# Optimization experiments

Hardware: AMD Instinct MI355X
Metric: run time of the kernel (lower is better)

Reference implementation:

```python
import jax, jax.numpy as jnp
import numpy as np

D_MODEL = 256
NHEAD = 8
HEAD_DIM = D_MODEL // NHEAD
TOP_K = 16
TEMP = 0.1
INF = 1e9
LAYER_NAMES = ['self', 'cross'] * 4


def _ln(x, g, b):
    m = jnp.mean(x, -1, keepdims=True)
    v = jnp.mean((x - m) ** 2, -1, keepdims=True)
    return (x - m) * jax.lax.rsqrt(v + 1e-5) * g + b


def _conf(f0, f1, m0, m1):
    # feats scaled by 1/sqrt(C) each, then /temperature -> sim / (C * TEMP)
    c = f0.shape[-1]
    sim = jnp.einsum('nlc,nsc->nls', f0, f1) / (c * TEMP)
    valid = m0[:, :, None] & m1[:, None, :]
    sim = jnp.where(valid, sim, -INF)
    return jax.nn.softmax(sim, axis=1) * jax.nn.softmax(sim, axis=2)


def _select(feat, conf, k):
    _, idx = jax.lax.top_k(conf, k)                 # [N, L, K]
    return jax.vmap(lambda f, i: f[i])(feat, idx)    # [N, L, K, C]


def _lin_attn(q, k, v, qm):
    # LoFTR LinearAttention: elu feature map, kv_mask is None here
    Q = jax.nn.elu(q) + 1.0
    K = jax.nn.elu(k) + 1.0
    if qm is not None:
        Q = Q * qm[:, :, None, None]
    vlen = v.shape[1]
    v = v / vlen
    KV = jnp.einsum('nshd,nshv->nhdv', K, v)
    Z = 1.0 / (jnp.einsum('nlhd,nhd->nlh', Q, K.sum(1)) + 1e-6)
    return jnp.einsum('nlhd,nhdv,nlh->nlhv', Q, KV, Z) * vlen


def _layer(x, src, xm, p):
    Wq, Wk, Wv, Wm, W1, W2, g1, b1, g2, b2 = p
    bs = x.shape[0]
    q = (x @ Wq).reshape(bs, -1, NHEAD, HEAD_DIM)
    k = (src @ Wk).reshape(bs, -1, NHEAD, HEAD_DIM)
    v = (src @ Wv).reshape(bs, -1, NHEAD, HEAD_DIM)
    msg = _lin_attn(q, k, v, xm)
    msg = msg.reshape(bs, -1, D_MODEL) @ Wm
    msg = _ln(msg, g1, b1)
    msg = jax.nn.relu(jnp.concatenate([x, msg], -1) @ W1) @ W2
    msg = _ln(msg, g2, b2)
    return x + msg


def _forward(feat0, feat1, mask0, mask1, Wq, Wk, Wv, Wm, W1, W2, g1, b1, g2, b2):
    N, L, C = feat0.shape
    S = feat1.shape[1]
    K = TOP_K
    m0f = mask0.reshape(N * L, 1).astype(feat0.dtype)
    m1f = mask1.reshape(N * S, 1).astype(feat0.dtype)
    for i, name in enumerate(LAYER_NAMES):
        p = (Wq[i], Wk[i], Wv[i], Wm[i], W1[i], W2[i], g1[i], b1[i], g2[i], b2[i])
        f0 = feat0.reshape(N * L, 1, C)
        f1 = feat1.reshape(N * S, 1, C)
        if name == 'self':
            s00 = _select(feat0, _conf(feat0, feat0, mask0, mask0), K).reshape(N * L, K, C)
            s11 = _select(feat1, _conf(feat1, feat1, mask1, mask1), K).reshape(N * S, K, C)
            feat0 = _layer(f0, s00, m0f, p).reshape(N, L, C)
            feat1 = _layer(f1, s11, m1f, p).reshape(N, S, C)
        else:
            c01 = _conf(feat0, feat1, mask0, mask1)
            s01 = _select(feat1, c01, K).reshape(N * L, K, C)
            s10 = _select(feat0, jnp.swapaxes(c01, 1, 2), K).reshape(N * S, K, C)
            feat0 = _layer(f0, s01, m0f, p).reshape(N, L, C)
            feat1 = _layer(f1, s10, m1f, p).reshape(N, S, C)
    return feat0, feat1


def setup_inputs() -> dict:
    key = jax.random.key(0)
    ks = jax.random.split(key, 10)
    N, L, S, C = 2, 4800, 4800, D_MODEL
    nl = len(LAYER_NAMES)
    w = 0.05
    return {
        'feat0': jax.random.normal(ks[0], (N, L, C), jnp.float32),
        'feat1': jax.random.normal(ks[1], (N, S, C), jnp.float32),
        'mask0': jnp.ones((N, L), jnp.bool_),
        'mask1': jnp.ones((N, S), jnp.bool_),
        'Wq': jax.random.normal(ks[2], (nl, C, C), jnp.float32) * w,
        'Wk': jax.random.normal(ks[3], (nl, C, C), jnp.float32) * w,
        'Wv': jax.random.normal(ks[4], (nl, C, C), jnp.float32) * w,
        'Wm': jax.random.normal(ks[5], (nl, C, C), jnp.float32) * w,
        'W1': jax.random.normal(ks[6], (nl, 2 * C, 2 * C), jnp.float32) * w,
        'W2': jax.random.normal(ks[7], (nl, 2 * C, C), jnp.float32) * w,
        'g1': jnp.ones((nl, C), jnp.float32),
        'b1': jnp.zeros((nl, C), jnp.float32),
        'g2': jnp.ones((nl, C), jnp.float32),
        'b2': jnp.zeros((nl, C), jnp.float32),
    }


def reference(feat0, feat1, mask0, mask1, Wq, Wk, Wv, Wm, W1, W2, g1, b1, g2, b2):
    return _forward(feat0, feat1, mask0, mask1, Wq, Wk, Wv, Wm, W1, W2, g1, b1, g2, b2)
```

## Files before the change

kernel.cpp:

```cpp
#include <hip/hip_runtime.h>

#define LLEN 4800
#define CDIM 256
#define NCH 8
#define CHROWS 600
#define SUBR 75

template <int MODE>
__global__ __launch_bounds__(256) void gemm_nt_sim(
    const float* __restrict__ A, const float* __restrict__ B,
    float* __restrict__ C, float* __restrict__ CT)
{
  const int bxi = blockIdx.x, byi = blockIdx.y;
  if (MODE == 1 && bxi < byi) return;
  const int bm = byi * 128, bn = bxi * 128;
  __shared__ float pool[MODE ? 8512 : 4224];
  float (*As)[132] = (float (*)[132])pool;
  float (*Bs)[132] = (float (*)[132])(pool + 2112);
  const int t = threadIdx.x;
  const int tx = t & 15, ty = t >> 4;
  const int lr = t >> 2, lk = (t & 3) * 4;
  float acc[8][8] = {};
  for (int k0 = 0; k0 < CDIM; k0 += 16) {
#pragma unroll
    for (int h = 0; h < 2; ++h) {
      const int row = lr + h * 64;
      const int ga = min(bm + row, LLEN - 1);
      const int gb = min(bn + row, LLEN - 1);
      const float4 a = *(const float4*)&A[(size_t)ga * CDIM + k0 + lk];
      const float4 b = *(const float4*)&B[(size_t)gb * CDIM + k0 + lk];
      As[lk + 0][row] = a.x; As[lk + 1][row] = a.y;
      As[lk + 2][row] = a.z; As[lk + 3][row] = a.w;
      Bs[lk + 0][row] = b.x; Bs[lk + 1][row] = b.y;
      Bs[lk + 2][row] = b.z; Bs[lk + 3][row] = b.w;
    }
    __syncthreads();
#pragma unroll
    for (int k = 0; k < 16; ++k) {
      const float4 a0 = *(const float4*)&As[k][ty * 4];
      const float4 a1 = *(const float4*)&As[k][64 + ty * 4];
      const float4 b0 = *(const float4*)&Bs[k][tx * 4];
      const float4 b1 = *(const float4*)&Bs[k][64 + tx * 4];
      const float av[8] = {a0.x, a0.y, a0.z, a0.w, a1.x, a1.y, a1.z, a1.w};
      const float bv[8] = {b0.x, b0.y, b0.z, b0.w, b1.x, b1.y, b1.z, b1.w};
#pragma unroll
      for (int i = 0; i < 8; ++i)
#pragma unroll
        for (int j = 0; j < 8; ++j) acc[i][j] += av[i] * bv[j];
    }
    __syncthreads();
  }
  const float sc = 1.f / 25.6f;
#pragma unroll
  for (int i = 0; i < 8; ++i) {
    const int row = bm + ((i < 4) ? ty * 4 + i : 64 + ty * 4 + (i - 4));
    if (row < LLEN) {
      const int c0 = bn + tx * 4;
      if (c0 < LLEN) {
        float4 o = {acc[i][0] * sc, acc[i][1] * sc, acc[i][2] * sc, acc[i][3] * sc};
        *(float4*)(C + (size_t)row * LLEN + c0) = o;
      }
      if (c0 + 64 < LLEN) {
        float4 o = {acc[i][4] * sc, acc[i][5] * sc, acc[i][6] * sc, acc[i][7] * sc};
        *(float4*)(C + (size_t)row * LLEN + c0 + 64) = o;
      }
    }
  }
  if (MODE == 0) return;
  if (MODE == 1 && bxi == byi) return;
  float* D = (MODE == 1) ? C : CT;
  float (*Ts)[133] = (float (*)[133])pool;
  for (int chunk = 0; chunk < 2; ++chunk) {
    __syncthreads();
#pragma unroll
    for (int i = 0; i < 8; ++i) {
      const int rl = (i < 4) ? ty * 4 + i : 64 + ty * 4 + (i - 4);
#pragma unroll
      for (int jj = 0; jj < 4; ++jj)
        Ts[tx * 4 + jj][rl] = acc[i][chunk * 4 + jj] * sc;
    }
    __syncthreads();
    const int cl = t >> 2, seg = t & 3;
    const int drow = bn + chunk * 64 + cl;
    if (drow < LLEN) {
#pragma unroll
      for (int q = 0; q < 8; ++q) {
        const int dcol = bm + seg * 32 + q * 4;
        if (dcol < LLEN) {
          const int b = seg * 32 + q * 4;
          float4 o = {Ts[cl][b], Ts[cl][b + 1], Ts[cl][b + 2], Ts[cl][b + 3]};
          *(float4*)(D + (size_t)drow * LLEN + dcol) = o;
        }
      }
    }
  }
}

template <int ACT>
__global__ __launch_bounds__(256) void gemm_nn(
    const float* __restrict__ A1, const float* __restrict__ A2,
    const float* __restrict__ B, float* __restrict__ C, int N, int K, int KA1)
{
  const int bm = blockIdx.y * 128, bn = blockIdx.x * 128;
  __shared__ float As[16][132];
  __shared__ float Bs[16][132];
  const int t = threadIdx.x;
  const int tx = t & 15, ty = t >> 4;
  const int lr = t >> 2, lk = (t & 3) * 4;
  const int bc = (t & 31) * 4, bk = t >> 5;
  float acc[8][8] = {};
  for (int k0 = 0; k0 < K; k0 += 16) {
    const float* Ap; int kloc, lda;
    if (k0 < KA1) { Ap = A1; kloc = k0; lda = KA1; }
    else          { Ap = A2; kloc = k0 - KA1; lda = K - KA1; }
#pragma unroll
    for (int h = 0; h < 2; ++h) {
      const int row = lr + h * 64;
      const float4 a = *(const float4*)&Ap[(size_t)(bm + row) * lda + kloc + lk];
      As[lk + 0][row] = a.x; As[lk + 1][row] = a.y;
      As[lk + 2][row] = a.z; As[lk + 3][row] = a.w;
    }
#pragma unroll
    for (int h = 0; h < 2; ++h) {
      const int kr = bk + h * 8;
      *(float4*)&Bs[kr][bc] = *(const float4*)&B[(size_t)(k0 + kr) * N + bn + bc];
    }
    __syncthreads();
#pragma unroll
    for (int k = 0; k < 16; ++k) {
      const float4 a0 = *(const float4*)&As[k][ty * 4];
      const float4 a1 = *(const float4*)&As[k][64 + ty * 4];
      const float4 b0 = *(const float4*)&Bs[k][tx * 4];
      const float4 b1 = *(const float4*)&Bs[k][64 + tx * 4];
      const float av[8] = {a0.x, a0.y, a0.z, a0.w, a1.x, a1.y, a1.z, a1.w};
      const float bv[8] = {b0.x, b0.y, b0.z, b0.w, b1.x, b1.y, b1.z, b1.w};
#pragma unroll
      for (int i = 0; i < 8; ++i)
#pragma unroll
        for (int j = 0; j < 8; ++j) acc[i][j] += av[i] * bv[j];
    }
    __syncthreads();
  }
#pragma unroll
  for (int i = 0; i < 8; ++i) {
    const int row = bm + ((i < 4) ? ty * 4 + i : 64 + ty * 4 + (i - 4));
    float4 o0 = {acc[i][0], acc[i][1], acc[i][2], acc[i][3]};
    float4 o1 = {acc[i][4], acc[i][5], acc[i][6], acc[i][7]};
    if (ACT == 1) {
      o0.x = fmaxf(o0.x, 0.f); o0.y = fmaxf(o0.y, 0.f);
      o0.z = fmaxf(o0.z, 0.f); o0.w = fmaxf(o0.w, 0.f);
      o1.x = fmaxf(o1.x, 0.f); o1.y = fmaxf(o1.y, 0.f);
      o1.z = fmaxf(o1.z, 0.f); o1.w = fmaxf(o1.w, 0.f);
    }
    *(float4*)(C + (size_t)row * N + bn + tx * 4) = o0;
    *(float4*)(C + (size_t)row * N + bn + tx * 4 + 64) = o1;
  }
}

__global__ __launch_bounds__(256) void gemm_qkv(
    const float* __restrict__ F,
    const float* __restrict__ Wq, const float* __restrict__ Wk, const float* __restrict__ Wv,
    float* __restrict__ qb, float* __restrict__ kb, float* __restrict__ vb)
{
  const int bm = blockIdx.y * 128;
  const int gn = blockIdx.x * 128;
  const int sel = gn >> 8;
  const int bn = gn & 255;
  const float* __restrict__ B = (sel == 0) ? Wq : (sel == 1) ? Wk : Wv;
  float* __restrict__ C = (sel == 0) ? qb : (sel == 1) ? kb : vb;
  __shared__ float As[16][132];
  __shared__ float Bs[16][132];
  const int t = threadIdx.x;
  const int tx = t & 15, ty = t >> 4;
  const int lr = t >> 2, lk = (t & 3) * 4;
  const int bc = (t & 31) * 4, bk = t >> 5;
  float acc[8][8] = {};
  for (int k0 = 0; k0 < CDIM; k0 += 16) {
#pragma unroll
    for (int h = 0; h < 2; ++h) {
      const int row = lr + h * 64;
      const float4 a = *(const float4*)&F[(size_t)(bm + row) * CDIM + k0 + lk];
      As[lk + 0][row] = a.x; As[lk + 1][row] = a.y;
      As[lk + 2][row] = a.z; As[lk + 3][row] = a.w;
    }
#pragma unroll
    for (int h = 0; h < 2; ++h) {
      const int kr = bk + h * 8;
      *(float4*)&Bs[kr][bc] = *(const float4*)&B[(size_t)(k0 + kr) * CDIM + bn + bc];
    }
    __syncthreads();
#pragma unroll
    for (int k = 0; k < 16; ++k) {
      const float4 a0 = *(const float4*)&As[k][ty * 4];
      const float4 a1 = *(const float4*)&As[k][64 + ty * 4];
      const float4 b0 = *(const float4*)&Bs[k][tx * 4];
      const float4 b1 = *(const float4*)&Bs[k][64 + tx * 4];
      const float av[8] = {a0.x, a0.y, a0.z, a0.w, a1.x, a1.y, a1.z, a1.w};
      const float bv[8] = {b0.x, b0.y, b0.z, b0.w, b1.x, b1.y, b1.z, b1.w};
#pragma unroll
      for (int i = 0; i < 8; ++i)
#pragma unroll
        for (int j = 0; j < 8; ++j) acc[i][j] += av[i] * bv[j];
    }
    __syncthreads();
  }
#pragma unroll
  for (int i = 0; i < 8; ++i) {
    const int row = bm + ((i < 4) ? ty * 4 + i : 64 + ty * 4 + (i - 4));
    float4 o0 = {acc[i][0], acc[i][1], acc[i][2], acc[i][3]};
    float4 o1 = {acc[i][4], acc[i][5], acc[i][6], acc[i][7]};
    *(float4*)(C + (size_t)row * CDIM + bn + tx * 4) = o0;
    *(float4*)(C + (size_t)row * CDIM + bn + tx * 4 + 64) = o1;
  }
}

__global__ __launch_bounds__(256) void row_stats(
    const float* __restrict__ sim, float* __restrict__ rowAdj)
{
  const int r = blockIdx.x;
  const float* row = sim + (size_t)r * LLEN;
  const int t = threadIdx.x;
  float m = -3e38f, s = 0.f;
  for (int j = t; j < LLEN; j += 256) {
    float x = row[j];
    if (x > m) { s = s * __expf(m - x) + 1.f; m = x; }
    else s += __expf(x - m);
  }
  __shared__ float sMax[256];
  __shared__ float sSum[256];
  sMax[t] = m; sSum[t] = s;
  __syncthreads();
  for (int off = 128; off > 0; off >>= 1) {
    if (t < off) {
      float m2 = sMax[t + off], s2 = sSum[t + off];
      float mm = fmaxf(sMax[t], m2);
      sSum[t] = sSum[t] * __expf(sMax[t] - mm) + s2 * __expf(m2 - mm);
      sMax[t] = mm;
    }
    __syncthreads();
  }
  if (t == 0) rowAdj[r] = sMax[0] + __logf(sSum[0]);
}

__global__ __launch_bounds__(256) void col_stats(
    const float* __restrict__ sim, float* __restrict__ partM, float* __restrict__ partS)
{
  const int t = threadIdx.x;
  const int c = t & 31, sub = t >> 5;
  const int s = blockIdx.x * 32 + c;
  const int ch = blockIdx.y;
  float m = -3e38f, sum = 0.f;
  const int l0 = ch * CHROWS + sub * SUBR;
  for (int l = l0; l < l0 + SUBR; ++l) {
    const float x = sim[(size_t)l * LLEN + s];
    if (x > m) { sum = sum * __expf(m - x) + 1.f; m = x; }
    else sum += __expf(x - m);
  }
  __shared__ float lm[8][32];
  __shared__ float ls[8][32];
  lm[sub][c] = m; ls[sub][c] = sum;
  __syncthreads();
  if (sub == 0) {
    float M = -3e38f, S = 0.f;
#pragma unroll
    for (int u = 0; u < 8; ++u) {
      const float m2 = lm[u][c], s2 = ls[u][c];
      const float mm = fmaxf(M, m2);
      S = S * __expf(M - mm) + s2 * __expf(m2 - mm);
      M = mm;
    }
    partM[(size_t)ch * LLEN + s] = M;
    partS[(size_t)ch * LLEN + s] = S;
  }
}

__global__ __launch_bounds__(256) void col_comb_stats(
    const float* __restrict__ partM, const float* __restrict__ partS,
    float* __restrict__ colAdj)
{
  const int s = blockIdx.x * 256 + threadIdx.x;
  if (s >= LLEN) return;
  float m = -3e38f, sum = 0.f;
#pragma unroll
  for (int ch = 0; ch < NCH; ++ch) {
    const float m2 = partM[(size_t)ch * LLEN + s], s2 = partS[(size_t)ch * LLEN + s];
    const float mm = fmaxf(m, m2);
    sum = sum * __expf(m - mm) + s2 * __expf(m2 - mm);
    m = mm;
  }
  colAdj[s] = m + __logf(sum);
}

__global__ __launch_bounds__(256, 4) void topk_fast(
    const float* __restrict__ M, const float* __restrict__ adj,
    int* __restrict__ idxOut, int kvOff)
{
  const int r = blockIdx.x;
  const float* row = M + (size_t)r * LLEN;
  const int t = threadIdx.x, lane = t & 63, w = t >> 6;
  __shared__ float keys[256 * 19];
  float lm = -3e38f; int la = 0;
#pragma unroll
  for (int j = 0; j < 19; ++j) {
    const int s = t + (j << 8);
    const float k = (s < LLEN) ? 2.f * row[s] - adj[s] : -3e38f;
    keys[t * 19 + j] = k;
    if (k > lm) { lm = k; la = j; }
  }
  __shared__ float wvv[4][16];
  __shared__ int   wii[4][16];
  for (int rnd = 0; rnd < 16; ++rnd) {
    float bv = lm;
    int   bs = (la << 8) + t;
#pragma unroll
    for (int off = 32; off; off >>= 1) {
      const float ov = __shfl_xor(bv, off);
      const int   os = __shfl_xor(bs, off);
      if (ov > bv || (ov == bv && os < bs)) { bv = ov; bs = os; }
    }
    if (lane == 0) { wvv[w][rnd] = bv; wii[w][rnd] = bs; }
    if (t == (bs & 255)) {
      keys[t * 19 + (bs >> 8)] = -3e38f;
      lm = -3e38f; la = 0;
#pragma unroll
      for (int j = 0; j < 19; ++j) {
        const float k = keys[t * 19 + j];
        if (k > lm) { lm = k; la = j; }
      }
    }
  }
  __syncthreads();
  if (w == 0) {
    float v = wvv[lane >> 4][lane & 15];
    const int s = wii[lane >> 4][lane & 15];
    for (int rnd = 0; rnd < 16; ++rnd) {
      float bv = v; int bl = lane;
#pragma unroll
      for (int off = 32; off; off >>= 1) {
        const float ov = __shfl_xor(bv, off);
        const int   ol = __shfl_xor(bl, off);
        if (ov > bv || (ov == bv && ol < bl)) { bv = ov; bl = ol; }
      }
      const int sw = __shfl(s, bl);
      if (lane == 0) idxOut[(size_t)r * 16 + rnd] = kvOff + sw;
      if (lane == bl) v = -3e38f;
    }
  }
}

__global__ __launch_bounds__(256) void attn_kernel(
    float* __restrict__ qb, const float* __restrict__ kb,
    const float* __restrict__ vb, const int* __restrict__ idx, int nTok)
{
  const int w = threadIdx.x >> 6, lane = threadIdx.x & 63;
  const int tok = blockIdx.x * 4 + w;
  if (tok >= nTok) return;
  const float4 qv = ((const float4*)(qb + (size_t)tok * CDIM))[lane];
  float Q[4];
  Q[0] = qv.x > 0.f ? qv.x + 1.f : __expf(qv.x);
  Q[1] = qv.y > 0.f ? qv.y + 1.f : __expf(qv.y);
  Q[2] = qv.z > 0.f ? qv.z + 1.f : __expf(qv.z);
  Q[3] = qv.w > 0.f ? qv.w + 1.f : __expf(qv.w);
  const int* ir = idx + (size_t)tok * 16;
  float mc[4] = {0.f, 0.f, 0.f, 0.f};
  float z = 0.f;
  for (int j = 0; j < 16; ++j) {
    const int src = ir[j];
    const float4 kv = ((const float4*)(kb + (size_t)src * CDIM))[lane];
    float p = Q[0] * (kv.x > 0.f ? kv.x + 1.f : __expf(kv.x))
            + Q[1] * (kv.y > 0.f ? kv.y + 1.f : __expf(kv.y))
            + Q[2] * (kv.z > 0.f ? kv.z + 1.f : __expf(kv.z))
            + Q[3] * (kv.w > 0.f ? kv.w + 1.f : __expf(kv.w));
    p += __shfl_xor(p, 1);
    p += __shfl_xor(p, 2);
    p += __shfl_xor(p, 4);
    const float4 vv = ((const float4*)(vb + (size_t)src * CDIM))[lane];
    mc[0] += p * vv.x; mc[1] += p * vv.y; mc[2] += p * vv.z; mc[3] += p * vv.w;
    z += p;
  }
  const float Z = 1.f / (z + 1e-6f);
  float4 o;
  o.x = mc[0] * Z; o.y = mc[1] * Z; o.z = mc[2] * Z; o.w = mc[3] * Z;
  ((float4*)(qb + (size_t)tok * CDIM))[lane] = o;
}

__global__ __launch_bounds__(256) void ln_inplace(
    float* __restrict__ x, const float* __restrict__ g, const float* __restrict__ b,
    int rows)
{
  const int w = threadIdx.x >> 6, lane = threadIdx.x & 63;
  const int r = blockIdx.x * 4 + w;
  if (r >= rows) return;
  float4 v = ((const float4*)(x + (size_t)r * CDIM))[lane];
  float s = v.x + v.y + v.z + v.w;
  float ss = v.x * v.x + v.y * v.y + v.z * v.z + v.w * v.w;
#pragma unroll
  for (int off = 1; off < 64; off <<= 1) {
    s += __shfl_xor(s, off);
    ss += __shfl_xor(ss, off);
  }
  const float mean = s * (1.f / CDIM);
  const float var = ss * (1.f / CDIM) - mean * mean;
  const float rstd = rsqrtf(var + 1e-5f);
  const float4 gv = ((const float4*)g)[lane];
  const float4 bv = ((const float4*)b)[lane];
  float4 o;
  o.x = (v.x - mean) * rstd * gv.x + bv.x;
  o.y = (v.y - mean) * rstd * gv.y + bv.y;
  o.z = (v.z - mean) * rstd * gv.z + bv.z;
  o.w = (v.w - mean) * rstd * gv.w + bv.w;
  ((float4*)(x + (size_t)r * CDIM))[lane] = o;
}

__global__ __launch_bounds__(256) void ln_res_kernel(
    const float* __restrict__ m2, const float* __restrict__ xin,
    const float* __restrict__ g, const float* __restrict__ b,
    float* __restrict__ out, int rows)
{
  const int w = threadIdx.x >> 6, lane = threadIdx.x & 63;
  const int r = blockIdx.x * 4 + w;
  if (r >= rows) return;
  const float4 v = ((const float4*)(m2 + (size_t)r * CDIM))[lane];
  float s = v.x + v.y + v.z + v.w;
  float ss = v.x * v.x + v.y * v.y + v.z * v.z + v.w * v.w;
#pragma unroll
  for (int off = 1; off < 64; off <<= 1) {
    s += __shfl_xor(s, off);
    ss += __shfl_xor(ss, off);
  }
  const float mean = s * (1.f / CDIM);
  const float var = ss * (1.f / CDIM) - mean * mean;
  const float rstd = rsqrtf(var + 1e-5f);
  const float4 gv = ((const float4*)g)[lane];
  const float4 bv = ((const float4*)b)[lane];
  const float4 xv = ((const float4*)(xin + (size_t)r * CDIM))[lane];
  float4 o;
  o.x = xv.x + (v.x - mean) * rstd * gv.x + bv.x;
  o.y = xv.y + (v.y - mean) * rstd * gv.y + bv.y;
  o.z = xv.z + (v.z - mean) * rstd * gv.z + bv.z;
  o.w = xv.w + (v.w - mean) * rstd * gv.w + bv.w;
  ((float4*)(out + (size_t)r * CDIM))[lane] = o;
}

extern "C" void kernel_launch(void* const* d_in, const int* in_sizes, int n_in,
                              void* d_out, int out_size, void* d_ws, size_t ws_size,
                              hipStream_t stream)
{
  (void)in_sizes; (void)n_in; (void)out_size;
  const float* in0 = (const float*)d_in[0];
  const float* in1 = (const float*)d_in[1];
  const float* Wq = (const float*)d_in[4];
  const float* Wk = (const float*)d_in[5];
  const float* Wv = (const float*)d_in[6];
  const float* Wm = (const float*)d_in[7];
  const float* W1 = (const float*)d_in[8];
  const float* W2 = (const float*)d_in[9];
  const float* g1 = (const float*)d_in[10];
  const float* b1 = (const float*)d_in[11];
  const float* g2 = (const float*)d_in[12];
  const float* b2 = (const float*)d_in[13];

  const size_t SIMF   = (size_t)LLEN * LLEN;
  const size_t SIDEQ  = (size_t)9600 * CDIM;
  const size_t NEED_F = SIMF + 4800 + 4800 + 2 * (size_t)NCH * LLEN
                      + 2 * (size_t)NCH * LLEN * 16 + (size_t)19200 * 16;
  if (ws_size < NEED_F * sizeof(float)) return;
  const bool haveT = (ws_size >= (NEED_F + SIMF) * sizeof(float));

  float* ws = (float*)d_ws;
  float* sim    = ws;
  float* rowAdj = ws + SIMF;
  float* colAdj = rowAdj + 4800;
  float* partM  = colAdj + 4800;
  float* partS  = partM + (size_t)NCH * LLEN;
  float* candV  = partS + (size_t)NCH * LLEN;
  int*   idxb   = (int*)(candV + 2 * (size_t)NCH * LLEN * 16);
  float* simT   = ws + NEED_F;

  float* qb = sim;
  float* kb = sim + 2 * SIDEQ;
  float* vb = sim + 4 * SIDEQ;
  float* hb = sim + 6 * SIDEQ;
  float* m2 = kb;
  float* mw = vb;

  const size_t fstride = (size_t)LLEN * CDIM;
  float* fA0 = (float*)d_out;
  float* fA1 = (float*)d_out + 2 * fstride;

  const float* cF0 = in0;
  const float* cF1 = in1;

  for (int i = 0; i < 8; ++i) {
    const bool isSelf = ((i & 1) == 0);
    const float* Wq_i = Wq + (size_t)i * CDIM * CDIM;
    const float* Wk_i = Wk + (size_t)i * CDIM * CDIM;
    const float* Wv_i = Wv + (size_t)i * CDIM * CDIM;
    const float* Wm_i = Wm + (size_t)i * CDIM * CDIM;
    const float* W1_i = W1 + (size_t)i * 512 * 512;
    const float* W2_i = W2 + (size_t)i * 512 * CDIM;
    const float* g1_i = g1 + (size_t)i * CDIM;
    const float* b1_i = b1 + (size_t)i * CDIM;
    const float* g2_i = g2 + (size_t)i * CDIM;
    const float* b2_i = b2 + (size_t)i * CDIM;

    if (isSelf) {
      for (int side = 0; side < 2; ++side) {
        const float* F = side ? cF1 : cF0;
        for (int n = 0; n < 2; ++n) {
          const float* Fn = F + (size_t)n * fstride;
          gemm_nt_sim<1><<<dim3(38, 38), 256, 0, stream>>>(Fn, Fn, sim, sim);
          row_stats<<<LLEN, 256, 0, stream>>>(sim, rowAdj);
          topk_fast<<<LLEN, 256, 0, stream>>>(
              sim, rowAdj, idxb + ((size_t)side * 9600 + (size_t)n * LLEN) * 16,
              side * 9600 + n * LLEN);
        }
      }
    } else {
      for (int n = 0; n < 2; ++n) {
        const float* F0n = cF0 + (size_t)n * fstride;
        const float* F1n = cF1 + (size_t)n * fstride;
        if (haveT) {
          gemm_nt_sim<2><<<dim3(38, 38), 256, 0, stream>>>(F0n, F1n, sim, simT);
          row_stats<<<LLEN, 256, 0, stream>>>(sim, rowAdj);
          col_stats<<<dim3(150, NCH), 256, 0, stream>>>(sim, partM, partS);
          col_comb_stats<<<dim3(19), 256, 0, stream>>>(partM, partS, colAdj);
          topk_fast<<<LLEN, 256, 0, stream>>>(
              sim, colAdj, idxb + ((size_t)n * LLEN) * 16, 9600 + n * LLEN);
          topk_fast<<<LLEN, 256, 0, stream>>>(
              simT, rowAdj, idxb + ((size_t)9600 + (size_t)n * LLEN) * 16, n * LLEN);
        } else {
          gemm_nt_sim<0><<<dim3(38, 38), 256, 0, stream>>>(F0n, F1n, sim, nullptr);
          row_stats<<<LLEN, 256, 0, stream>>>(sim, rowAdj);
          col_stats<<<dim3(150, NCH), 256, 0, stream>>>(sim, partM, partS);
          col_comb_stats<<<dim3(19), 256, 0, stream>>>(partM, partS, colAdj);
          topk_fast<<<LLEN, 256, 0, stream>>>(
              sim, colAdj, idxb + ((size_t)n * LLEN) * 16, 9600 + n * LLEN);
          gemm_nt_sim<0><<<dim3(38, 38), 256, 0, stream>>>(F1n, F0n, sim, nullptr);
          topk_fast<<<LLEN, 256, 0, stream>>>(
              sim, rowAdj, idxb + ((size_t)9600 + (size_t)n * LLEN) * 16, n * LLEN);
        }
      }
    }

    for (int side = 0; side < 2; ++side) {
      const float* F = side ? cF1 : cF0;
      const size_t ob = (size_t)side * SIDEQ;
      gemm_qkv<<<dim3(6, 75), 256, 0, stream>>>(
          F, Wq_i, Wk_i, Wv_i, qb + ob, kb + ob, vb + ob);
    }

    for (int side = 0; side < 2; ++side)
      attn_kernel<<<2400, 256, 0, stream>>>(
          qb + side * SIDEQ, kb, vb, idxb + (size_t)side * 9600 * 16, 9600);

    for (int side = 0; side < 2; ++side)
      gemm_nn<0><<<dim3(2, 75), 256, 0, stream>>>(
          qb + side * SIDEQ, nullptr, Wm_i, mw + side * SIDEQ, 256, 256, 256);
    ln_inplace<<<4800, 256, 0, stream>>>(mw, g1_i, b1_i, 19200);

    for (int side = 0; side < 2; ++side) {
      const float* F = side ? cF1 : cF0;
      gemm_nn<1><<<dim3(4, 75), 256, 0, stream>>>(
          F, mw + side * SIDEQ, W1_i, hb, 512, 512, 256);
      gemm_nn<0><<<dim3(2, 75), 256, 0, stream>>>(
          hb, nullptr, W2_i, m2 + side * SIDEQ, 256, 512, 512);
    }

    ln_res_kernel<<<2400, 256, 0, stream>>>(m2, cF0, g2_i, b2_i, fA0, 9600);
    ln_res_kernel<<<2400, 256, 0, stream>>>(m2 + SIDEQ, cF1, g2_i, b2_i, fA1, 9600);
    cF0 = fA0; cF1 = fA1;
  }
}
```

Baseline: 11.26 ms.

## Double GEMM k-tile depth, vectorize col_stats, and batch both sides per launch

The shared-memory K tile in all SGEMM kernels grows from 16 to 32, halving the number of sync-separated iterations but doubling LDS use, which may lower occupancy. col_stats now reads float4 per thread and covers 64 columns per 128-thread block. After the first layer, both sides are processed in single launches over the contiguous output buffer (QKV, attention, Wm, W1, W2, LN), cutting launch count and giving larger grids. The hidden buffer now holds both sides at once, so it needs more scratch memory.

```diff
diff --git a/kernel.cpp b/kernel.cpp
--- a/kernel.cpp
+++ b/kernel.cpp
@@ -14,17 +14,17 @@
   const int bxi = blockIdx.x, byi = blockIdx.y;
   if (MODE == 1 && bxi < byi) return;
   const int bm = byi * 128, bn = bxi * 128;
-  __shared__ float pool[MODE ? 8512 : 4224];
+  __shared__ float pool[MODE ? 8512 : 8448];
   float (*As)[132] = (float (*)[132])pool;
-  float (*Bs)[132] = (float (*)[132])(pool + 2112);
+  float (*Bs)[132] = (float (*)[132])(pool + 4224);
   const int t = threadIdx.x;
   const int tx = t & 15, ty = t >> 4;
-  const int lr = t >> 2, lk = (t & 3) * 4;
+  const int lr = t >> 3, lk = (t & 7) * 4;
   float acc[8][8] = {};
-  for (int k0 = 0; k0 < CDIM; k0 += 16) {
-#pragma unroll
-    for (int h = 0; h < 2; ++h) {
-      const int row = lr + h * 64;
+  for (int k0 = 0; k0 < CDIM; k0 += 32) {
+#pragma unroll
+    for (int h = 0; h < 4; ++h) {
+      const int row = lr + h * 32;
       const int ga = min(bm + row, LLEN - 1);
       const int gb = min(bn + row, LLEN - 1);
       const float4 a = *(const float4*)&A[(size_t)ga * CDIM + k0 + lk];
@@ -36,7 +36,7 @@
     }
     __syncthreads();
 #pragma unroll
-    for (int k = 0; k < 16; ++k) {
+    for (int k = 0; k < 32; ++k) {
       const float4 a0 = *(const float4*)&As[k][ty * 4];
       const float4 a1 = *(const float4*)&As[k][64 + ty * 4];
       const float4 b0 = *(const float4*)&Bs[k][tx * 4];
@@ -102,32 +102,32 @@
     const float* __restrict__ B, float* __restrict__ C, int N, int K, int KA1)
 {
   const int bm = blockIdx.y * 128, bn = blockIdx.x * 128;
-  __shared__ float As[16][132];
-  __shared__ float Bs[16][132];
+  __shared__ float As[32][132];
+  __shared__ float Bs[32][132];
   const int t = threadIdx.x;
   const int tx = t & 15, ty = t >> 4;
-  const int lr = t >> 2, lk = (t & 3) * 4;
+  const int lr = t >> 3, lk = (t & 7) * 4;
   const int bc = (t & 31) * 4, bk = t >> 5;
   float acc[8][8] = {};
-  for (int k0 = 0; k0 < K; k0 += 16) {
+  for (int k0 = 0; k0 < K; k0 += 32) {
     const float* Ap; int kloc, lda;
     if (k0 < KA1) { Ap = A1; kloc = k0; lda = KA1; }
     else          { Ap = A2; kloc = k0 - KA1; lda = K - KA1; }
 #pragma unroll
-    for (int h = 0; h < 2; ++h) {
-      const int row = lr + h * 64;
+    for (int h = 0; h < 4; ++h) {
+      const int row = lr + h * 32;
       const float4 a = *(const float4*)&Ap[(size_t)(bm + row) * lda + kloc + lk];
       As[lk + 0][row] = a.x; As[lk + 1][row] = a.y;
       As[lk + 2][row] = a.z; As[lk + 3][row] = a.w;
     }
 #pragma unroll
-    for (int h = 0; h < 2; ++h) {
+    for (int h = 0; h < 4; ++h) {
       const int kr = bk + h * 8;
       *(float4*)&Bs[kr][bc] = *(const float4*)&B[(size_t)(k0 + kr) * N + bn + bc];
     }
     __syncthreads();
 #pragma unroll
-    for (int k = 0; k < 16; ++k) {
+    for (int k = 0; k < 32; ++k) {
       const float4 a0 = *(const float4*)&As[k][ty * 4];
       const float4 a1 = *(const float4*)&As[k][64 + ty * 4];
       const float4 b0 = *(const float4*)&Bs[k][tx * 4];
@@ -168,29 +168,29 @@
   const int bn = gn & 255;
   const float* __restrict__ B = (sel == 0) ? Wq : (sel == 1) ? Wk : Wv;
   float* __restrict__ C = (sel == 0) ? qb : (sel == 1) ? kb : vb;
-  __shared__ float As[16][132];
-  __shared__ float Bs[16][132];
+  __shared__ float As[32][132];
+  __shared__ float Bs[32][132];
   const int t = threadIdx.x;
   const int tx = t & 15, ty = t >> 4;
-  const int lr = t >> 2, lk = (t & 3) * 4;
+  const int lr = t >> 3, lk = (t & 7) * 4;
   const int bc = (t & 31) * 4, bk = t >> 5;
   float acc[8][8] = {};
-  for (int k0 = 0; k0 < CDIM; k0 += 16) {
-#pragma unroll
-    for (int h = 0; h < 2; ++h) {
-      const int row = lr + h * 64;
+  for (int k0 = 0; k0 < CDIM; k0 += 32) {
+#pragma unroll
+    for (int h = 0; h < 4; ++h) {
+      const int row = lr + h * 32;
       const float4 a = *(const float4*)&F[(size_t)(bm + row) * CDIM + k0 + lk];
       As[lk + 0][row] = a.x; As[lk + 1][row] = a.y;
       As[lk + 2][row] = a.z; As[lk + 3][row] = a.w;
     }
 #pragma unroll
-    for (int h = 0; h < 2; ++h) {
+    for (int h = 0; h < 4; ++h) {
       const int kr = bk + h * 8;
       *(float4*)&Bs[kr][bc] = *(const float4*)&B[(size_t)(k0 + kr) * CDIM + bn + bc];
     }
     __syncthreads();
 #pragma unroll
-    for (int k = 0; k < 16; ++k) {
+    for (int k = 0; k < 32; ++k) {
       const float4 a0 = *(const float4*)&As[k][ty * 4];
       const float4 a1 = *(const float4*)&As[k][64 + ty * 4];
       const float4 b0 = *(const float4*)&Bs[k][tx * 4];
@@ -242,35 +242,45 @@
   if (t == 0) rowAdj[r] = sMax[0] + __logf(sSum[0]);
 }
 
-__global__ __launch_bounds__(256) void col_stats(
+__global__ __launch_bounds__(128) void col_stats(
     const float* __restrict__ sim, float* __restrict__ partM, float* __restrict__ partS)
 {
   const int t = threadIdx.x;
-  const int c = t & 31, sub = t >> 5;
-  const int s = blockIdx.x * 32 + c;
+  const int cg = t & 15, sub = t >> 4;
+  const int c0 = blockIdx.x * 64 + cg * 4;
   const int ch = blockIdx.y;
-  float m = -3e38f, sum = 0.f;
+  float m0 = -3e38f, m1 = -3e38f, m2 = -3e38f, m3 = -3e38f;
+  float s0 = 0.f, s1 = 0.f, s2 = 0.f, s3 = 0.f;
   const int l0 = ch * CHROWS + sub * SUBR;
   for (int l = l0; l < l0 + SUBR; ++l) {
-    const float x = sim[(size_t)l * LLEN + s];
-    if (x > m) { sum = sum * __expf(m - x) + 1.f; m = x; }
-    else sum += __expf(x - m);
-  }
-  __shared__ float lm[8][32];
-  __shared__ float ls[8][32];
-  lm[sub][c] = m; ls[sub][c] = sum;
+    const float4 x = *(const float4*)&sim[(size_t)l * LLEN + c0];
+    if (x.x > m0) { s0 = s0 * __expf(m0 - x.x) + 1.f; m0 = x.x; } else s0 += __expf(x.x - m0);
+    if (x.y > m1) { s1 = s1 * __expf(m1 - x.y) + 1.f; m1 = x.y; } else s1 += __expf(x.y - m1);
+    if (x.z > m2) { s2 = s2 * __expf(m2 - x.z) + 1.f; m2 = x.z; } else s2 += __expf(x.z - m2);
+    if (x.w > m3) { s3 = s3 * __expf(m3 - x.w) + 1.f; m3 = x.w; } else s3 += __expf(x.w - m3);
+  }
+  __shared__ float lm[8][64];
+  __shared__ float ls[8][64];
+  lm[sub][cg * 4 + 0] = m0; ls[sub][cg * 4 + 0] = s0;
+  lm[sub][cg * 4 + 1] = m1; ls[sub][cg * 4 + 1] = s1;
+  lm[sub][cg * 4 + 2] = m2; ls[sub][cg * 4 + 2] = s2;
+  lm[sub][cg * 4 + 3] = m3; ls[sub][cg * 4 + 3] = s3;
   __syncthreads();
   if (sub == 0) {
-    float M = -3e38f, S = 0.f;
-#pragma unroll
-    for (int u = 0; u < 8; ++u) {
-      const float m2 = lm[u][c], s2 = ls[u][c];
-      const float mm = fmaxf(M, m2);
-      S = S * __expf(M - mm) + s2 * __expf(m2 - mm);
-      M = mm;
-    }
-    partM[(size_t)ch * LLEN + s] = M;
-    partS[(size_t)ch * LLEN + s] = S;
+#pragma unroll
+    for (int j = 0; j < 4; ++j) {
+      const int c = cg * 4 + j;
+      float M = -3e38f, S = 0.f;
+#pragma unroll
+      for (int u = 0; u < 8; ++u) {
+        const float mm2 = lm[u][c], ss2 = ls[u][c];
+        const float mm = fmaxf(M, mm2);
+        S = S * __expf(M - mm) + ss2 * __expf(mm2 - mm);
+        M = mm;
+      }
+      partM[(size_t)ch * LLEN + c0 + j] = M;
+      partS[(size_t)ch * LLEN + c0 + j] = S;
+    }
   }
 }
 
@@ -480,7 +490,7 @@
   float* qb = sim;
   float* kb = sim + 2 * SIDEQ;
   float* vb = sim + 4 * SIDEQ;
-  float* hb = sim + 6 * SIDEQ;
+  float* hbF = sim + 6 * SIDEQ;
   float* m2 = kb;
   float* mw = vb;
 
@@ -523,7 +533,7 @@
         if (haveT) {
           gemm_nt_sim<2><<<dim3(38, 38), 256, 0, stream>>>(F0n, F1n, sim, simT);
           row_stats<<<LLEN, 256, 0, stream>>>(sim, rowAdj);
-          col_stats<<<dim3(150, NCH), 256, 0, stream>>>(sim, partM, partS);
+          col_stats<<<dim3(75, NCH), 128, 0, stream>>>(sim, partM, partS);
           col_comb_stats<<<dim3(19), 256, 0, stream>>>(partM, partS, colAdj);
           topk_fast<<<LLEN, 256, 0, stream>>>(
               sim, colAdj, idxb + ((size_t)n * LLEN) * 16, 9600 + n * LLEN);
@@ -532,7 +542,7 @@
         } else {
           gemm_nt_sim<0><<<dim3(38, 38), 256, 0, stream>>>(F0n, F1n, sim, nullptr);
           row_stats<<<LLEN, 256, 0, stream>>>(sim, rowAdj);
-          col_stats<<<dim3(150, NCH), 256, 0, stream>>>(sim, partM, partS);
+          col_stats<<<dim3(75, NCH), 128, 0, stream>>>(sim, partM, partS);
           col_comb_stats<<<dim3(19), 256, 0, stream>>>(partM, partS, colAdj);
           topk_fast<<<LLEN, 256, 0, stream>>>(
               sim, colAdj, idxb + ((size_t)n * LLEN) * 16, 9600 + n * LLEN);
@@ -543,32 +553,42 @@
       }
     }
 
-    for (int side = 0; side < 2; ++side) {
-      const float* F = side ? cF1 : cF0;
-      const size_t ob = (size_t)side * SIDEQ;
-      gemm_qkv<<<dim3(6, 75), 256, 0, stream>>>(
-          F, Wq_i, Wk_i, Wv_i, qb + ob, kb + ob, vb + ob);
-    }
-
-    for (int side = 0; side < 2; ++side)
-      attn_kernel<<<2400, 256, 0, stream>>>(
-          qb + side * SIDEQ, kb, vb, idxb + (size_t)side * 9600 * 16, 9600);
-
-    for (int side = 0; side < 2; ++side)
-      gemm_nn<0><<<dim3(2, 75), 256, 0, stream>>>(
-          qb + side * SIDEQ, nullptr, Wm_i, mw + side * SIDEQ, 256, 256, 256);
+    if (i == 0) {
+      for (int side = 0; side < 2; ++side) {
+        const float* F = side ? cF1 : cF0;
+        const size_t ob = (size_t)side * SIDEQ;
+        gemm_qkv<<<dim3(6, 75), 256, 0, stream>>>(
+            F, Wq_i, Wk_i, Wv_i, qb + ob, kb + ob, vb + ob);
+      }
+    } else {
+      gemm_qkv<<<dim3(6, 150), 256, 0, stream>>>(
+          (const float*)d_out, Wq_i, Wk_i, Wv_i, qb, kb, vb);
+    }
+
+    attn_kernel<<<4800, 256, 0, stream>>>(qb, kb, vb, idxb, 19200);
+
+    gemm_nn<0><<<dim3(2, 150), 256, 0, stream>>>(qb, nullptr, Wm_i, mw, 256, 256, 256);
     ln_inplace<<<4800, 256, 0, stream>>>(mw, g1_i, b1_i, 19200);
 
-    for (int side = 0; side < 2; ++side) {
-      const float* F = side ? cF1 : cF0;
-      gemm_nn<1><<<dim3(4, 75), 256, 0, stream>>>(
-          F, mw + side * SIDEQ, W1_i, hb, 512, 512, 256);
-      gemm_nn<0><<<dim3(2, 75), 256, 0, stream>>>(
-          hb, nullptr, W2_i, m2 + side * SIDEQ, 256, 512, 512);
-    }
-
-    ln_res_kernel<<<2400, 256, 0, stream>>>(m2, cF0, g2_i, b2_i, fA0, 9600);
-    ln_res_kernel<<<2400, 256, 0, stream>>>(m2 + SIDEQ, cF1, g2_i, b2_i, fA1, 9600);
+    if (i == 0) {
+      for (int side = 0; side < 2; ++side) {
+        const float* F = side ? cF1 : cF0;
+        gemm_nn<1><<<dim3(4, 75), 256, 0, stream>>>(
+            F, mw + side * SIDEQ, W1_i, hbF + (size_t)side * 9600 * 512, 512, 512, 256);
+      }
+    } else {
+      gemm_nn<1><<<dim3(4, 150), 256, 0, stream>>>(
+          (const float*)d_out, mw, W1_i, hbF, 512, 512, 256);
+    }
+    gemm_nn<0><<<dim3(2, 150), 256, 0, stream>>>(hbF, nullptr, W2_i, m2, 256, 512, 512);
+
+    if (i == 0) {
+      ln_res_kernel<<<2400, 256, 0, stream>>>(m2, cF0, g2_i, b2_i, fA0, 9600);
+      ln_res_kernel<<<2400, 256, 0, stream>>>(m2 + SIDEQ, cF1, g2_i, b2_i, fA1, 9600);
+    } else {
+      ln_res_kernel<<<4800, 256, 0, stream>>>(
+          m2, (const float*)d_out, g2_i, b2_i, (float*)d_out, 19200);
+    }
     cF0 = fA0; cF1 = fA1;
   }
 }
```

Result: faster. 10.39 ms (-7.7%).
